# Kernel optimization log

Hardware: AMD Instinct MI355X
Metric: run time of the kernel (lower is better)

## Reference

```python
import jax, jax.numpy as jnp
import numpy as np


def setup_inputs() -> dict:
    key = jax.random.key(0)
    k1, k2 = jax.random.split(key)
    B, C, H, W = 16, 64, 512, 512
    x = jax.random.normal(k1, (B, C, H, W), dtype=jnp.float32)
    mask = jax.random.randint(k2, (B, 1, H, W), 0, 2, dtype=jnp.int32)
    return {"x": x, "mask": mask}


def reference(x, mask):
    # x: (B, C, H, W); mask: (B, 1, H, W) with 0/1 entries. pool_type == 'max'.
    m = (mask != 0)[:, 0]                              # (B, H, W) boolean
    # masked max over spatial positions; excluded positions -> -inf
    masked = jnp.where(m[:, None, :, :], x, -jnp.inf)   # (B, C, H, W)
    pooled = jnp.max(masked, axis=(2, 3))               # (B, C)
    count = jnp.sum(m, axis=(1, 2))                     # (B,)
    # batches with empty mask produce zeros (torch code skips them)
    return jnp.where((count > 0)[:, None], pooled, jnp.zeros_like(pooled))
```

## Files before the change

kernel.cpp:

```cpp
#include <hip/hip_runtime.h>
#include <math.h>

#define BB 16
#define CC 64
#define HW (512 * 512)
#define SS 8
#define CH (HW / SS)
#define TPB 256
#define VEC_ITERS (CH / 4 / TPB)

__global__ __launch_bounds__(TPB) void maskpool_partial(
    const float* __restrict__ x,
    const int* __restrict__ mask,
    float* __restrict__ partial) {
  const int blk = blockIdx.x;
  const int b = blk / (SS * CC);
  const int rem = blk % (SS * CC);
  const int s = rem / CC;
  const int c = rem % CC;

  const float4* __restrict__ xp = reinterpret_cast<const float4*>(
      x + (size_t)(b * CC + c) * HW + (size_t)s * CH);
  const int4* __restrict__ mp = reinterpret_cast<const int4*>(
      mask + (size_t)b * HW + (size_t)s * CH);

  const int t = threadIdx.x;
  float acc = -INFINITY;

#pragma unroll 4
  for (int i = 0; i < VEC_ITERS; ++i) {
    const float4 xv = xp[t + i * TPB];
    const int4 mv = mp[t + i * TPB];
    acc = fmaxf(acc, mv.x ? xv.x : -INFINITY);
    acc = fmaxf(acc, mv.y ? xv.y : -INFINITY);
    acc = fmaxf(acc, mv.z ? xv.z : -INFINITY);
    acc = fmaxf(acc, mv.w ? xv.w : -INFINITY);
  }

#pragma unroll
  for (int off = 32; off > 0; off >>= 1)
    acc = fmaxf(acc, __shfl_down(acc, off));

  __shared__ float wred[TPB / 64];
  const int wave = t >> 6;
  if ((t & 63) == 0) wred[wave] = acc;
  __syncthreads();
  if (t == 0) {
    float m = fmaxf(fmaxf(wred[0], wred[1]), fmaxf(wred[2], wred[3]));
    partial[(size_t)(b * CC + c) * SS + s] = m;
  }
}

__global__ __launch_bounds__(TPB) void maskpool_final(
    const float* __restrict__ partial, float* __restrict__ out) {
  const int tid = blockIdx.x * blockDim.x + threadIdx.x;
  if (tid < BB * CC) {
    float m = -INFINITY;
#pragma unroll
    for (int s = 0; s < SS; ++s) m = fmaxf(m, partial[(size_t)tid * SS + s]);
    out[tid] = (m == -INFINITY) ? 0.0f : m;
  }
}

extern "C" void kernel_launch(void* const* d_in, const int* in_sizes, int n_in,
                              void* d_out, int out_size, void* d_ws,
                              size_t ws_size, hipStream_t stream) {
  const float* x = (const float*)d_in[0];
  const int* mask = (const int*)d_in[1];
  float* out = (float*)d_out;
  float* partial = (float*)d_ws;

  const int nblk1 = BB * CC * SS;
  maskpool_partial<<<nblk1, TPB, 0, stream>>>(x, mask, partial);

  const int nblk2 = (BB * CC + TPB - 1) / TPB;
  maskpool_final<<<nblk2, TPB, 0, stream>>>(partial, out);
}
```

Measured before the change: 1.327 ms.

## Pack mask into 4-bit bytes and use nontemporal loads for x

Adds a pre-pass kernel that compresses the int32 mask into one byte per four elements, stored in workspace. The main reduction reads these packed bytes instead of int4 mask vectors, cutting the mask traffic that every channel block re-reads. It also streams x with nontemporal loads and increases the unroll. The cost is an extra kernel launch and a dependency on the workspace having room past the partial buffer.

Result: faster. 1.276 ms (-3.9%).

```diff
diff --git a/kernel.cpp b/kernel.cpp
--- a/kernel.cpp
+++ b/kernel.cpp
@@ -8,10 +8,23 @@
 #define CH (HW / SS)
 #define TPB 256
 #define VEC_ITERS (CH / 4 / TPB)
+#define GROUPS (BB * HW / 4)
+#define PM_PER_B (HW / 4)
+#define PM_CH (CH / 4)
+
+typedef float f4 __attribute__((ext_vector_type(4)));
+
+__global__ __launch_bounds__(TPB) void mask_pack(
+    const int4* __restrict__ mask, unsigned char* __restrict__ pm) {
+  const int g = blockIdx.x * TPB + threadIdx.x;
+  const int4 m = mask[g];
+  pm[g] = (unsigned char)((m.x != 0) | ((m.y != 0) << 1) |
+                          ((m.z != 0) << 2) | ((m.w != 0) << 3));
+}
 
 __global__ __launch_bounds__(TPB) void maskpool_partial(
     const float* __restrict__ x,
-    const int* __restrict__ mask,
+    const unsigned char* __restrict__ pm,
     float* __restrict__ partial) {
   const int blk = blockIdx.x;
   const int b = blk / (SS * CC);
@@ -19,22 +32,23 @@
   const int s = rem / CC;
   const int c = rem % CC;
 
-  const float4* __restrict__ xp = reinterpret_cast<const float4*>(
+  const f4* __restrict__ xp = reinterpret_cast<const f4*>(
       x + (size_t)(b * CC + c) * HW + (size_t)s * CH);
-  const int4* __restrict__ mp = reinterpret_cast<const int4*>(
-      mask + (size_t)b * HW + (size_t)s * CH);
+  const unsigned char* __restrict__ mp =
+      pm + (size_t)b * PM_PER_B + (size_t)s * PM_CH;
 
   const int t = threadIdx.x;
   float acc = -INFINITY;
 
-#pragma unroll 4
+#pragma unroll 8
   for (int i = 0; i < VEC_ITERS; ++i) {
-    const float4 xv = xp[t + i * TPB];
-    const int4 mv = mp[t + i * TPB];
-    acc = fmaxf(acc, mv.x ? xv.x : -INFINITY);
-    acc = fmaxf(acc, mv.y ? xv.y : -INFINITY);
-    acc = fmaxf(acc, mv.z ? xv.z : -INFINITY);
-    acc = fmaxf(acc, mv.w ? xv.w : -INFINITY);
+    const int idx = t + i * TPB;
+    const f4 xv = __builtin_nontemporal_load(xp + idx);
+    const unsigned int mb = mp[idx];
+    acc = fmaxf(acc, (mb & 1u) ? xv.x : -INFINITY);
+    acc = fmaxf(acc, (mb & 2u) ? xv.y : -INFINITY);
+    acc = fmaxf(acc, (mb & 4u) ? xv.z : -INFINITY);
+    acc = fmaxf(acc, (mb & 8u) ? xv.w : -INFINITY);
   }
 
 #pragma unroll
@@ -69,9 +83,13 @@
   const int* mask = (const int*)d_in[1];
   float* out = (float*)d_out;
   float* partial = (float*)d_ws;
+  unsigned char* pm = (unsigned char*)d_ws + 32768;
+
+  const int nblk0 = GROUPS / TPB;
+  mask_pack<<<nblk0, TPB, 0, stream>>>((const int4*)mask, pm);
 
   const int nblk1 = BB * CC * SS;
-  maskpool_partial<<<nblk1, TPB, 0, stream>>>(x, mask, partial);
+  maskpool_partial<<<nblk1, TPB, 0, stream>>>(x, pm, partial);
 
   const int nblk2 = (BB * CC + TPB - 1) / TPB;
   maskpool_final<<<nblk2, TPB, 0, stream>>>(partial, out);
```
